# Performance work log

Measured on AMD Instinct MI355X. Metric: run time of the kernel, lower is better.

The kernel has to match this reference:

```python
import jax, jax.numpy as jnp
import numpy as np

N_SAMPLES = 2 ** 15  # 32768
NYQUIST = 22050.0 / 2.0
MIN_FREQ = 40.0 / NYQUIST
MAX_FREQ = 4000.0 / NYQUIST
FREQ_RANGE = MAX_FREQ - MIN_FREQ


def interp_linear(x, out_size):
    """torch F.interpolate(mode='linear', align_corners=False) along last axis."""
    in_size = x.shape[-1]
    scale = in_size / out_size
    coords = (jnp.arange(out_size, dtype=x.dtype) + 0.5) * scale - 0.5
    coords = jnp.clip(coords, 0.0, in_size - 1)
    lo = jnp.floor(coords).astype(jnp.int32)
    hi = jnp.minimum(lo + 1, in_size - 1)
    w = coords - lo.astype(x.dtype)
    return x[..., lo] * (1.0 - w) + x[..., hi] * w


def translate(pair, shift, scale):
    # angle of complex(pair[:,:,0], pair[:,:,1]) / pi, then affine
    angle = jnp.arctan2(pair[:, :, 1, :], pair[:, :, 0, :]) / np.pi
    return shift + angle * scale


def setup_inputs() -> dict:
    key = jax.random.key(0)
    k1, k2 = jax.random.split(key)
    x = jax.random.normal(k1, (16, 8, 10, 128), dtype=jnp.float32)
    noise = jax.random.normal(k2, (16, 8, N_SAMPLES), dtype=jnp.float32)
    return {"x": x, "noise": noise}


def reference(x, noise):
    # x: (batch, n_osc, 10, time_ctrl); noise: (batch, n_osc, N_SAMPLES)
    basic = x[:, :, 0:2, :]
    amp = jnp.sqrt(jnp.sum(basic * basic, axis=2))            # (b, o, t)
    amp = interp_linear(amp, N_SAMPLES)                       # (b, o, N)

    f0 = translate(basic, MIN_FREQ, FREQ_RANGE)               # control-rate
    mix = interp_linear(translate(x[:, :, 2:4, :], 1.0, 0.5), N_SAMPLES)
    harm_amp = amp * mix
    noise_amp = amp * (1.0 - mix)

    noise_std = translate(x[:, :, 4:6, :], MIN_FREQ, FREQ_RANGE)
    mod_factor = translate(x[:, :, 6:8, :], 0.25, 4.75)
    b = translate(x[:, :, 8:10, :], 0.1, 9.9)

    # band_filtered_noise: narrowband noise as a frequency-jittered sine
    f0_fr = interp_linear(f0, N_SAMPLES)
    std_fr = interp_linear(noise_std, N_SAMPLES)
    bfn = jnp.sin(jnp.cumsum(f0_fr + noise * std_fr, axis=-1))
    noise_sig = noise_amp * bfn

    mod_factor = interp_linear(mod_factor, N_SAMPLES)
    b = interp_linear(b, N_SAMPLES)
    mod = b * jnp.sin(jnp.cumsum(mod_factor, axis=-1))
    sig = harm_amp * jnp.sin(jnp.cumsum(f0_fr, axis=-1) + mod)

    mixed = noise_sig + sig                                   # (b, o, N)
    return jnp.mean(mixed, axis=1, keepdims=True)             # (b, 1, N)
```

## Files before the change

### kernel.cpp

```cpp
#include <hip/hip_runtime.h>
#include <math.h>

#define NS      32768
#define NB      128
#define NSEQ    128
#define NCHUNK  256
#define CHUNK   128
#define CELL    16
#define PART    512
#define NPARTS  (NS / PART)
#define TPB     256
#define NBATCH  16
#define NBIN    4
#define SJ      ((CELL * (CELL - 1)) / 2)

__device__ __forceinline__ float sinr(float x) {
    return __builtin_amdgcn_sinf(x - rintf(x));
}

__device__ __forceinline__ void seg_params_f(int i, int& lo, int& hi,
                                             float& w0, float& wst) {
    if (i < 128)            { lo = 0;   hi = 1;   w0 = 0.f; wst = 0.f; }
    else if (i >= NS - 128) { lo = 127; hi = 127; w0 = 0.f; wst = 0.f; }
    else {
        lo = (i - 128) >> 8;  hi = lo + 1;
        int off = (i - 128) & 255;
        w0 = (float)(off + 0.5f) * (1.0f / 256.0f);
        wst = 1.0f / 256.0f;
    }
}

__device__ __forceinline__ double bin_value(const float* xs, int q, int j) {
    const double PI_    = 3.14159265358979323846;
    const double INV2PI = 0.15915494309189533576888376337251;
    const double MINF   = 40.0 / 11025.0;
    const double FRNG   = (4000.0 - 40.0) / 11025.0;
    if (q == 0) {
        double a0 = (double)xs[j], a1 = (double)xs[NB + j];
        return sqrt(a0 * a0 + a1 * a1);
    }
    double ang = atan2((double)xs[(2 * q - 1) * NB + j],
                       (double)xs[(2 * q - 2) * NB + j]) / PI_;
    double sh, sc;
    if      (q == 1) { sh = MINF; sc = FRNG; }
    else if (q == 2) { sh = 1.0;  sc = 0.5;  }
    else if (q == 3) { sh = MINF; sc = FRNG; }
    else if (q == 4) { sh = 0.25; sc = 4.75; }
    else             { sh = 0.1;  sc = 9.9;  }
    double v = sh + ang * sc;
    if (q != 2) v *= INV2PI;
    return v;
}

__global__ __launch_bounds__(TPB)
void sum_kernel(const float* __restrict__ ng, float* __restrict__ chunkS) {
    int bid = blockIdx.x;
    int seq = bid >> 5, blk = bid & 31;
    int t = threadIdx.x;
    int ck = t >> 5, l = t & 31;
    int base = blk * 1024 + ck * CHUNK + l * 4;
    const float4 nv = *reinterpret_cast<const float4*>(
        ng + (size_t)seq * NS + base);
    float j0 = (float)(l * 4);
    float s0 = nv.x + nv.y + nv.z + nv.w;
    float s1 = fmaf(j0, nv.x, fmaf(j0 + 1.f, nv.y,
               fmaf(j0 + 2.f, nv.z, (j0 + 3.f) * nv.w)));
    #pragma unroll
    for (int m = 1; m <= 16; m <<= 1) {
        s0 += __shfl_xor(s0, m);
        s1 += __shfl_xor(s1, m);
    }
    if (l == 0) {
        int chunk = blk * 8 + ck;
        float2* o = reinterpret_cast<float2*>(
            chunkS + ((size_t)seq * NCHUNK + chunk) * 2);
        *o = make_float2(s0, s1);
    }
}

__global__ __launch_bounds__(TPB)
void anchor_kernel(const float* __restrict__ xg, const float* __restrict__ chunkS,
                   float* __restrict__ binsG, float* __restrict__ frG) {
    __shared__ double bf[3][NB];
    __shared__ double wsum[4][3];

    int seq = blockIdx.x;
    int t = threadIdx.x;
    const float* xs = xg + (size_t)seq * 10 * NB;

    for (int idx = t; idx < 6 * NB; idx += TPB) {
        int q = idx >> 7, j = idx & (NB - 1);
        double v = bin_value(xs, q, j);
        binsG[((size_t)seq * 6 + q) * NB + j] = (float)v;
        if      (q == 1) bf[0][j] = v;
        else if (q == 3) bf[1][j] = v;
        else if (q == 4) bf[2][j] = v;
    }
    __syncthreads();

    int c = t;
    float2 sv = *reinterpret_cast<const float2*>(
        chunkS + ((size_t)seq * NCHUNK + c) * 2);
    double S0 = (double)sv.x, S1 = (double)sv.y;
    double t1, t3, t2;
    if (c == 0) {
        t3 = 128.0 * bf[0][0];
        t2 = 128.0 * bf[2][0];
        t1 = t3 + bf[1][0] * S0;
    } else if (c == NCHUNK - 1) {
        t3 = 128.0 * bf[0][NB - 1];
        t2 = 128.0 * bf[2][NB - 1];
        t1 = t3 + bf[1][NB - 1] * S0;
    } else {
        int k = (c - 1) >> 1, hf = (c - 1) & 1;
        double sw  = 64.0 * (double)hf + 32.0;
        double f0L = bf[0][k], dF0 = bf[0][k + 1] - f0L;
        double stL = bf[1][k], dSt = bf[1][k + 1] - stL;
        double mfL = bf[2][k], dMf = bf[2][k + 1] - mfL;
        t3 = 128.0 * f0L + dF0 * sw;
        t2 = 128.0 * mfL + dMf * sw;
        t1 = t3 + stL * S0
                + dSt * ((128.0 * (double)hf + 0.5) * S0 + S1) * (1.0 / 256.0);
    }

    int lane = t & 63, wid = t >> 6;
    double v1 = t1, v3 = t3, v2 = t2;
    #pragma unroll
    for (int d = 1; d < 64; d <<= 1) {
        double u1 = __shfl_up(v1, d);
        double u3 = __shfl_up(v3, d);
        double u2 = __shfl_up(v2, d);
        if (lane >= d) { v1 += u1; v3 += u3; v2 += u2; }
    }
    if (lane == 63) { wsum[wid][0] = v1; wsum[wid][1] = v3; wsum[wid][2] = v2; }
    __syncthreads();
    double b1 = 0.0, b3 = 0.0, b2 = 0.0;
    #pragma unroll
    for (int k = 0; k < 3; ++k)
        if (wid > k) { b1 += wsum[k][0]; b3 += wsum[k][1]; b2 += wsum[k][2]; }
    v1 += b1; v3 += b3; v2 += b2;

    if ((c & 3) == 3 && c < 4 * (NPARTS - 1)) {
        int p = (c >> 2) + 1;
        float* o = frG + ((size_t)seq * NPARTS + p) * 3;
        o[0] = (float)(v1 - rint(v1));
        o[1] = (float)(v3 - rint(v3));
        o[2] = (float)(v2 - rint(v2));
    }
    if (c == 0) {
        float* o = frG + (size_t)seq * NPARTS * 3;
        o[0] = 0.f; o[1] = 0.f; o[2] = 0.f;
    }
}

__global__ __launch_bounds__(TPB, 4)
void fm_kernel(const float* __restrict__ ng, const float* __restrict__ binsG,
               const float* __restrict__ frG, float* __restrict__ out) {
    __shared__ float binsB[8][6][NBIN];
    __shared__ float frL[8][3];
    __shared__ float wtot[4][8][3];

    int bx = blockIdx.x;
    int bb = bx >> 6, p = bx & (NPARTS - 1);
    int tid = threadIdx.x, lane = tid & 63, wid = tid >> 6;
    int h = tid & 7, c = tid >> 3;
    int P = p * PART;
    int b0 = (P - 128) >> 8; if (b0 < 0) b0 = 0;
    int s  = (bb << 3) + h;
    int i0 = P + c * CELL;

    const float4* np_ = reinterpret_cast<const float4*>(ng + (size_t)s * NS + i0);
    float4 nv[CELL / 4];
    #pragma unroll
    for (int q4 = 0; q4 < CELL / 4; ++q4) nv[q4] = np_[q4];

    if (tid < 192) {
        int j = tid & 3, q = (tid >> 2) % 6, h2 = tid / 24;
        binsB[h2][q][j] =
            binsG[((size_t)((bb << 3) + h2) * 6 + q) * NB + min(b0 + j, NB - 1)];
    }
    if (tid < 24) {
        int k = tid % 3, h2 = tid / 3;
        frL[h2][k] = frG[((size_t)((bb << 3) + h2) * NPARTS + p) * 3 + k];
    }
    __syncthreads();

    int lo, hi; float w0, wst;
    seg_params_f(i0, lo, hi, w0, wst);
    int jL = lo - b0, jH = hi - b0;

    float amL = binsB[h][0][jL], dAm = binsB[h][0][jH] - amL;
    float g0L = binsB[h][1][jL], gF0 = binsB[h][1][jH] - g0L;
    float mxL = binsB[h][2][jL], dMx = binsB[h][2][jH] - mxL;
    float gsL = binsB[h][3][jL], gSt = binsB[h][3][jH] - gsL;
    float gmL = binsB[h][4][jL], gMf = binsB[h][4][jH] - gmL;
    float bbL = binsB[h][5][jL], dBb = binsB[h][5][jH] - bbL;

    float s0 = 0.f, s1 = 0.f;
    #pragma unroll
    for (int q4 = 0; q4 < CELL / 4; ++q4) {
        float jd = (float)(q4 * 4);
        s0 += nv[q4].x; s1 = fmaf(jd,       nv[q4].x, s1);
        s0 += nv[q4].y; s1 = fmaf(jd + 1.f, nv[q4].y, s1);
        s0 += nv[q4].z; s1 = fmaf(jd + 2.f, nv[q4].z, s1);
        s0 += nv[q4].w; s1 = fmaf(jd + 3.f, nv[q4].w, s1);
    }
    float sw = (float)CELL * w0 + (float)SJ * wst;
    float t3 = (float)CELL * g0L + gF0 * sw;
    float t2 = (float)CELL * gmL + gMf * sw;
    float t1 = t3 + gsL * s0 + gSt * fmaf(w0, s0, wst * s1);

    float v1 = t1, v3 = t3, v2 = t2;
    #pragma unroll
    for (int d = 8; d < 64; d <<= 1) {
        float u1 = __shfl_up(v1, d);
        float u3 = __shfl_up(v3, d);
        float u2 = __shfl_up(v2, d);
        if (lane >= d) { v1 += u1; v3 += u3; v2 += u2; }
    }
    if (lane >= 56) { wtot[wid][h][0] = v1; wtot[wid][h][1] = v3; wtot[wid][h][2] = v2; }
    __syncthreads();
    float b1 = 0.f, b3 = 0.f, b2 = 0.f;
    #pragma unroll
    for (int k = 0; k < 3; ++k)
        if (wid > k) { b1 += wtot[k][h][0]; b3 += wtot[k][h][1]; b2 += wtot[k][h][2]; }

    float fr1 = frL[h][0] + b1 + (v1 - t1); fr1 -= rintf(fr1);
    float fr3 = frL[h][1] + b3 + (v3 - t3); fr3 -= rintf(fr3);
    float fr2 = frL[h][2] + b2 + (v2 - t2); fr2 -= rintf(fr2);

    float arr[CELL];
    float d1 = 0.f, d2 = 0.f, d3 = 0.f;
    #pragma unroll
    for (int q4 = 0; q4 < CELL / 4; ++q4) {
        float nf[4] = {nv[q4].x, nv[q4].y, nv[q4].z, nv[q4].w};
        #pragma unroll
        for (int u = 0; u < 4; ++u) {
            int j = q4 * 4 + u;
            float wf  = fmaf((float)j, wst, w0);
            float f0v = fmaf(wf, gF0, g0L);
            float stv = fmaf(wf, gSt, gsL);
            float mfv = fmaf(wf, gMf, gmL);
            d3 += f0v;
            d1 += fmaf(nf[u], stv, f0v);
            d2 += mfv;
            float ampv = fmaf(wf, dAm, amL);
            float mixv = fmaf(wf, dMx, mxL);
            float bv   = fmaf(wf, dBb, bbL);
            float s2 = sinr(fr2 + d2);
            float sA = sinr(fr1 + d1);
            float sB = sinr(fmaf(bv, s2, fr3 + d3));
            float harm = ampv * mixv;
            arr[j] = fmaf(harm, sB, (ampv - harm) * sA);
        }
    }

    #pragma unroll
    for (int m = 1; m <= 4; m <<= 1) {
        #pragma unroll
        for (int j = 0; j < CELL; ++j) arr[j] += __shfl_xor(arr[j], m);
    }
    if (h == 0) {
        float4* op = reinterpret_cast<float4*>(out + (size_t)bb * NS + i0);
        #pragma unroll
        for (int j4 = 0; j4 < CELL / 4; ++j4)
            op[j4] = make_float4(arr[j4 * 4 + 0] * 0.125f, arr[j4 * 4 + 1] * 0.125f,
                                 arr[j4 * 4 + 2] * 0.125f, arr[j4 * 4 + 3] * 0.125f);
    }
}

extern "C" void kernel_launch(void* const* d_in, const int* in_sizes, int n_in,
                              void* d_out, int out_size, void* d_ws, size_t ws_size,
                              hipStream_t stream) {
    const float* x     = (const float*)d_in[0];
    const float* noise = (const float*)d_in[1];
    float* out = (float*)d_out;
    float* chunkS = (float*)d_ws;
    float* binsG  = (float*)((char*)d_ws + 262144);
    float* frG    = (float*)((char*)d_ws + 262144 + 393216);
    sum_kernel<<<NSEQ * 32, TPB, 0, stream>>>(noise, chunkS);
    anchor_kernel<<<NSEQ, TPB, 0, stream>>>(x, chunkS, binsG, frG);
    fm_kernel<<<NBATCH * NPARTS, TPB, 0, stream>>>(noise, binsG, frG, out);
}
```

Baseline: 81.57 us.

## Fuse noise chunk-sum pass into anchor kernel, dropping a launch

Removes the separate sum_kernel and has each thread of the anchor kernel compute its own chunk's plain and index-weighted noise sums directly. This eliminates one kernel launch and the workspace round trip for chunk sums. In exchange, the 16 MB noise read is done by only 128 blocks with strided per-thread access, which reduces memory parallelism and coalescing.

```diff
diff --git a/kernel.cpp b/kernel.cpp
--- a/kernel.cpp
+++ b/kernel.cpp
@@ -53,40 +53,27 @@
 }
 
 __global__ __launch_bounds__(TPB)
-void sum_kernel(const float* __restrict__ ng, float* __restrict__ chunkS) {
-    int bid = blockIdx.x;
-    int seq = bid >> 5, blk = bid & 31;
-    int t = threadIdx.x;
-    int ck = t >> 5, l = t & 31;
-    int base = blk * 1024 + ck * CHUNK + l * 4;
-    const float4 nv = *reinterpret_cast<const float4*>(
-        ng + (size_t)seq * NS + base);
-    float j0 = (float)(l * 4);
-    float s0 = nv.x + nv.y + nv.z + nv.w;
-    float s1 = fmaf(j0, nv.x, fmaf(j0 + 1.f, nv.y,
-               fmaf(j0 + 2.f, nv.z, (j0 + 3.f) * nv.w)));
-    #pragma unroll
-    for (int m = 1; m <= 16; m <<= 1) {
-        s0 += __shfl_xor(s0, m);
-        s1 += __shfl_xor(s1, m);
-    }
-    if (l == 0) {
-        int chunk = blk * 8 + ck;
-        float2* o = reinterpret_cast<float2*>(
-            chunkS + ((size_t)seq * NCHUNK + chunk) * 2);
-        *o = make_float2(s0, s1);
-    }
-}
-
-__global__ __launch_bounds__(TPB)
-void anchor_kernel(const float* __restrict__ xg, const float* __restrict__ chunkS,
-                   float* __restrict__ binsG, float* __restrict__ frG) {
+void pre_kernel(const float* __restrict__ xg, const float* __restrict__ ng,
+                float* __restrict__ binsG, float* __restrict__ frG) {
     __shared__ double bf[3][NB];
     __shared__ double wsum[4][3];
 
     int seq = blockIdx.x;
     int t = threadIdx.x;
     const float* xs = xg + (size_t)seq * 10 * NB;
+
+    const float4* np_ = reinterpret_cast<const float4*>(
+        ng + (size_t)seq * NS + (size_t)t * CHUNK);
+    float s0 = 0.f, s1 = 0.f;
+    #pragma unroll 8
+    for (int j = 0; j < CHUNK / 4; ++j) {
+        float4 v = np_[j];
+        float jd = (float)(j * 4);
+        s0 += v.x; s1 = fmaf(jd,       v.x, s1);
+        s0 += v.y; s1 = fmaf(jd + 1.f, v.y, s1);
+        s0 += v.z; s1 = fmaf(jd + 2.f, v.z, s1);
+        s0 += v.w; s1 = fmaf(jd + 3.f, v.w, s1);
+    }
 
     for (int idx = t; idx < 6 * NB; idx += TPB) {
         int q = idx >> 7, j = idx & (NB - 1);
@@ -99,9 +86,7 @@
     __syncthreads();
 
     int c = t;
-    float2 sv = *reinterpret_cast<const float2*>(
-        chunkS + ((size_t)seq * NCHUNK + c) * 2);
-    double S0 = (double)sv.x, S1 = (double)sv.y;
+    double S0 = (double)s0, S1 = (double)s1;
     double t1, t3, t2;
     if (c == 0) {
         t3 = 128.0 * bf[0][0];
@@ -275,10 +260,8 @@
     const float* x     = (const float*)d_in[0];
     const float* noise = (const float*)d_in[1];
     float* out = (float*)d_out;
-    float* chunkS = (float*)d_ws;
-    float* binsG  = (float*)((char*)d_ws + 262144);
-    float* frG    = (float*)((char*)d_ws + 262144 + 393216);
-    sum_kernel<<<NSEQ * 32, TPB, 0, stream>>>(noise, chunkS);
-    anchor_kernel<<<NSEQ, TPB, 0, stream>>>(x, chunkS, binsG, frG);
+    float* binsG = (float*)d_ws;
+    float* frG   = (float*)((char*)d_ws + 393216);
+    pre_kernel<<<NSEQ, TPB, 0, stream>>>(x, noise, binsG, frG);
     fm_kernel<<<NBATCH * NPARTS, TPB, 0, stream>>>(noise, binsG, frG, out);
 }
```

Result: no change. 80.44 us (-1.4%).
